# Performance work log

Measured on AMD Instinct MI355X. Metric: run time of the kernel, lower is better.

## Reference

```python
import jax, jax.numpy as jnp
import numpy as np

N = 20000        # nodes
E = 160000       # directed edges (before self loops)
NODE_DIM = 1287
HEADS = 4
C1, C2, C3 = 128, 256, 128
ACT_SLOPE = 0.15   # module's LeakyReLU between layers
GAT_SLOPE = 0.2    # PyG GATConv default negative_slope


def _gat_layer(x, src, dst, W, att_src, att_dst, bias, heads, out_dim, concat):
    # x: [N, in] ; W: [in, heads*out] ; att_*: [heads, out] ; bias: [heads*out] or [out]
    h = (x @ W).reshape(N, heads, out_dim)                      # [N, H, C]
    a_s = jnp.einsum('nhc,hc->nh', h, att_src)                  # [N, H]
    a_d = jnp.einsum('nhc,hc->nh', h, att_dst)                  # [N, H]
    e = jax.nn.leaky_relu(a_s[src] + a_d[dst], GAT_SLOPE)       # [Etot, H]
    # segment softmax over incoming edges of each dst node (self loops => no empty segments)
    m = jax.ops.segment_max(e, dst, num_segments=N)             # [N, H]
    w = jnp.exp(e - m[dst])
    den = jax.ops.segment_sum(w, dst, num_segments=N)           # [N, H]
    alpha = w / den[dst]                                        # [Etot, H]
    msg = h[src] * alpha[:, :, None]                            # [Etot, H, C]
    out = jax.ops.segment_sum(msg, dst, num_segments=N)         # [N, H, C]
    out = out.reshape(N, heads * out_dim) if concat else out.mean(axis=1)
    return out + bias


def setup_inputs() -> dict:
    key = jax.random.key(0)
    ks = jax.random.split(key, 22)
    s = 0.05
    x = jax.random.normal(ks[0], (N, NODE_DIM), jnp.float32)
    edge_index = jax.random.randint(ks[1], (2, E), 0, N, dtype=jnp.int64)
    inp = {
        'x': x, 'edge_index': edge_index,
        'W1': jax.random.normal(ks[2], (NODE_DIM, HEADS * C1), jnp.float32) * s,
        'as1': jax.random.normal(ks[3], (HEADS, C1), jnp.float32) * s,
        'ad1': jax.random.normal(ks[4], (HEADS, C1), jnp.float32) * s,
        'b1': jnp.zeros((HEADS * C1,), jnp.float32),
        'W2': jax.random.normal(ks[5], (HEADS * C1, HEADS * C2), jnp.float32) * s,
        'as2': jax.random.normal(ks[6], (HEADS, C2), jnp.float32) * s,
        'ad2': jax.random.normal(ks[7], (HEADS, C2), jnp.float32) * s,
        'b2': jnp.zeros((HEADS * C2,), jnp.float32),
        # conv3: 1024 -> 128, 1 head, no concat
        'W3': jax.random.normal(ks[8], (HEADS * C2, C3), jnp.float32) * s,
        'as3': jax.random.normal(ks[9], (1, C3), jnp.float32) * s,
        'ad3': jax.random.normal(ks[10], (1, C3), jnp.float32) * s,
        'b3': jnp.zeros((C3,), jnp.float32),
        # pre_fc: 128 -> 16
        'pw': jax.random.normal(ks[11], (C3, 16), jnp.float32) * s,
        'pb': jnp.zeros((16,), jnp.float32),
        # fc fallback: Linear(16,32) -> LeakyReLU(0.15) -> Linear(32,2)
        'f1w': jax.random.normal(ks[12], (16, 32), jnp.float32) * s,
        'f1b': jnp.zeros((32,), jnp.float32),
        'f2w': jax.random.normal(ks[13], (32, 2), jnp.float32) * s,
        'f2b': jnp.zeros((2,), jnp.float32),
    }
    return inp


def reference(x, edge_index, W1, as1, ad1, b1, W2, as2, ad2, b2,
              W3, as3, ad3, b3, pw, pb, f1w, f1b, f2w, f2b):
    loop = jnp.arange(N, dtype=edge_index.dtype)
    src = jnp.concatenate([edge_index[0], loop])   # PyG add_self_loops=True
    dst = jnp.concatenate([edge_index[1], loop])
    h = _gat_layer(x, src, dst, W1, as1, ad1, b1, HEADS, C1, True)
    h = jax.nn.leaky_relu(h, ACT_SLOPE)            # dropout = identity (eval)
    h = _gat_layer(h, src, dst, W2, as2, ad2, b2, HEADS, C2, True)
    h = jax.nn.leaky_relu(h, ACT_SLOPE)
    h = _gat_layer(h, src, dst, W3, as3, ad3, b3, 1, C3, False)
    h = jax.nn.leaky_relu(h, ACT_SLOPE)
    h = h @ pw + pb                                 # pre_fc (128 -> 16)
    h = jax.nn.leaky_relu(h @ f1w + f1b, ACT_SLOPE)
    return h @ f2w + f2b                            # [N, 2] logits
```

## Files before the change

### kernel.cpp

```cpp
#include <hip/hip_runtime.h>
#include <hip/hip_bf16.h>
#include <cstdint>
#include <cstddef>

#define LRELU(x, s) ((x) > 0.f ? (x) : (s) * (x))

typedef __attribute__((ext_vector_type(8))) short bf16x8;
typedef __attribute__((ext_vector_type(4))) float f32x4;

__device__ __forceinline__ float bflo(uint v) { return __uint_as_float(v << 16); }
__device__ __forceinline__ float bfhi(uint v) { return __uint_as_float(v & 0xffff0000u); }
__device__ __forceinline__ ushort f2bf(float f) {
  const uint u = __float_as_uint(f);
  return (ushort)((u + 0x7fffu + ((u >> 16) & 1u)) >> 16);
}

__device__ __forceinline__ void async16(const ushort* g, ushort* l) {
  __builtin_amdgcn_global_load_lds(
      (const __attribute__((address_space(1))) unsigned int*)g,
      (__attribute__((address_space(3))) unsigned int*)l, 16, 0, 0);
}

__global__ void cast_pad_rows(const float* __restrict__ in, ushort* __restrict__ out,
                              int rows, int K, int Kp) {
  const int P4 = Kp >> 2;
  const long long idx = (long long)blockIdx.x * blockDim.x + threadIdx.x;
  if (idx >= (long long)rows * P4) return;
  const int r = (int)(idx / P4);
  const int c = ((int)(idx - (long long)r * P4)) << 2;
  const float* p = in + (size_t)r * K + c;
  float v0 = 0.f, v1 = 0.f, v2 = 0.f, v3 = 0.f;
  if (c + 3 < K) { v0 = p[0]; v1 = p[1]; v2 = p[2]; v3 = p[3]; }
  else {
    if (c + 0 < K) v0 = p[0];
    if (c + 1 < K) v1 = p[1];
    if (c + 2 < K) v2 = p[2];
    if (c + 3 < K) v3 = p[3];
  }
  uint2 o;
  o.x = (uint)f2bf(v0) | ((uint)f2bf(v1) << 16);
  o.y = (uint)f2bf(v2) | ((uint)f2bf(v3) << 16);
  *(uint2*)(out + (size_t)r * Kp + c) = o;
}

__global__ void cast_W_T(const float* __restrict__ W, ushort* __restrict__ Wt,
                         int K, int Nn, int Kp) {
  __shared__ float tile[32][33];
  const int kt = blockIdx.x * 32;
  const int nt = blockIdx.y * 32;
  const int tx = threadIdx.x;
  const int ty = threadIdx.y;
  for (int r = ty; r < 32; r += 8) {
    const int k = kt + r, nn = nt + tx;
    tile[r][tx] = (k < K && nn < Nn) ? W[(size_t)k * Nn + nn] : 0.f;
  }
  __syncthreads();
  for (int r = ty; r < 32; r += 8) {
    const int nn = nt + r, k = kt + tx;
    if (nn < Nn && k < Kp) Wt[(size_t)nn * Kp + k] = f2bf(tile[tx][r]);
  }
}

__global__ __launch_bounds__(256) void gemm_bf16(
    const ushort* __restrict__ A, const ushort* __restrict__ Bt, ushort* __restrict__ C,
    int M, int N, int Kp,
    const float* __restrict__ AS, const float* __restrict__ AD,
    float* __restrict__ asb, float* __restrict__ adb, int H, int headC) {
  __shared__ ushort sA[128 * 32];
  __shared__ ushort sB[128 * 32];
  const int tid = threadIdx.x;
  const int wave = tid >> 6;
  const int lane = tid & 63;
  const int tilesN = N >> 7;
  const int bx = blockIdx.x % tilesN;
  const int by = blockIdx.x / tilesN;
  const int wrow = (wave >> 1) * 64;
  const int wcol = (wave & 1) * 64;
  const int quad = lane >> 4;
  const int ml = lane & 15;

  const int r0 = wave * 32 + (lane >> 2);
  const int r1 = r0 + 16;
  const int seg = (lane & 3) * 8;
  const int gA0 = min(by * 128 + r0, M - 1);
  const int gA1 = min(by * 128 + r1, M - 1);
  const int gB0 = bx * 128 + r0;
  const int gB1 = bx * 128 + r1;
  const ushort* pA0 = A + (size_t)gA0 * Kp + seg;
  const ushort* pA1 = A + (size_t)gA1 * Kp + seg;
  const ushort* pB0 = Bt + (size_t)gB0 * Kp + seg;
  const ushort* pB1 = Bt + (size_t)gB1 * Kp + seg;
  ushort* lA0 = &sA[(wave * 32) * 32];
  ushort* lA1 = &sA[(wave * 32 + 16) * 32];
  ushort* lB0 = &sB[(wave * 32) * 32];
  ushort* lB1 = &sB[(wave * 32 + 16) * 32];

  f32x4 acc[4][4];
#pragma unroll
  for (int mi = 0; mi < 4; mi++)
#pragma unroll
    for (int ni = 0; ni < 4; ni++)
#pragma unroll
      for (int e = 0; e < 4; e++) acc[mi][ni][e] = 0.f;

  for (int k0 = 0; k0 < Kp; k0 += 32) {
    __syncthreads();
    async16(pA0 + k0, lA0);
    async16(pA1 + k0, lA1);
    async16(pB0 + k0, lB0);
    async16(pB1 + k0, lB1);
    __syncthreads();
    bf16x8 af[4], bfr[4];
#pragma unroll
    for (int mi = 0; mi < 4; mi++)
      af[mi] = *(const bf16x8*)&sA[(wrow + mi * 16 + ml) * 32 + quad * 8];
#pragma unroll
    for (int ni = 0; ni < 4; ni++)
      bfr[ni] = *(const bf16x8*)&sB[(wcol + ni * 16 + ml) * 32 + quad * 8];
#pragma unroll
    for (int mi = 0; mi < 4; mi++)
#pragma unroll
      for (int ni = 0; ni < 4; ni++)
        acc[mi][ni] = __builtin_amdgcn_mfma_f32_16x16x32_bf16(af[mi], bfr[ni], acc[mi][ni], 0, 0, 0);
  }

#pragma unroll
  for (int mi = 0; mi < 4; mi++) {
#pragma unroll
    for (int r = 0; r < 4; r++) {
      const int row = by * 128 + wrow + mi * 16 + quad * 4 + r;
      if (row < M) {
#pragma unroll
        for (int ni = 0; ni < 4; ni++) {
          const int col = bx * 128 + wcol + ni * 16 + ml;
          C[(size_t)row * N + col] = f2bf(acc[mi][ni][r]);
        }
      }
    }
  }

  if (asb != nullptr) {
    float asv[4], adv[4];
#pragma unroll
    for (int ni = 0; ni < 4; ni++) {
      const int col = bx * 128 + wcol + ni * 16 + ml;
      asv[ni] = AS[col];
      adv[ni] = AD[col];
    }
    const int hh = (bx * 128 + wcol) / headC;
#pragma unroll
    for (int mi = 0; mi < 4; mi++) {
#pragma unroll
      for (int r = 0; r < 4; r++) {
        float ps = acc[mi][0][r] * asv[0] + acc[mi][1][r] * asv[1] +
                   acc[mi][2][r] * asv[2] + acc[mi][3][r] * asv[3];
        float pd = acc[mi][0][r] * adv[0] + acc[mi][1][r] * adv[1] +
                   acc[mi][2][r] * adv[2] + acc[mi][3][r] * adv[3];
#pragma unroll
        for (int off = 1; off < 16; off <<= 1) {
          ps += __shfl_xor(ps, off);
          pd += __shfl_xor(pd, off);
        }
        if (ml == 0) {
          const int row = by * 128 + wrow + mi * 16 + quad * 4 + r;
          if (row < M) {
            atomicAdd(&asb[row * H + hh], ps);
            atomicAdd(&adb[row * H + hh], pd);
          }
        }
      }
    }
  }
}

__global__ void count_deg(const int* __restrict__ dst, int E, int* __restrict__ deg) {
  const int t = blockIdx.x * blockDim.x + threadIdx.x;
  if (t < E) atomicAdd(&deg[dst[t]], 1);
}

__global__ __launch_bounds__(1024) void scan_kernel(const int* __restrict__ deg,
                                                    int* __restrict__ rowptr,
                                                    int* __restrict__ cursor, int n) {
  __shared__ int swsum[16];
  __shared__ int carry_s;
  const int t = threadIdx.x;
  const int wv = t >> 6, lane = t & 63;
  if (t == 0) carry_s = 0;
  __syncthreads();
  for (int base = 0; base < n; base += 1024) {
    const int i = base + t;
    const int v = (i < n) ? (deg[i] + 1) : 0;
    int sc = v;
#pragma unroll
    for (int off = 1; off < 64; off <<= 1) {
      const int u = __shfl_up(sc, off);
      if (lane >= off) sc += u;
    }
    if (lane == 63) swsum[wv] = sc;
    __syncthreads();
    if (t < 16) {
      int x = swsum[t];
#pragma unroll
      for (int off = 1; off < 16; off <<= 1) {
        const int u = __shfl_up(x, off);
        if (t >= off) x += u;
      }
      swsum[t] = x;
    }
    __syncthreads();
    const int incl = sc + (wv == 0 ? 0 : swsum[wv - 1]) + carry_s;
    if (i < n) { rowptr[i + 1] = incl; cursor[i] = incl - v; }
    if (base == 0 && t == 0) rowptr[0] = 0;
    __syncthreads();
    if (t == 0) carry_s += swsum[15];
    __syncthreads();
  }
}

__global__ void scatter_edges(const int* __restrict__ esrc, const int* __restrict__ edst,
                              int E, int Etot, int* __restrict__ cursor,
                              int* __restrict__ csr_src) {
  const int t = blockIdx.x * blockDim.x + threadIdx.x;
  if (t >= Etot) return;
  int s, d;
  if (t < E) { s = esrc[t]; d = edst[t]; } else { s = t - E; d = s; }
  const int pos = atomicAdd(&cursor[d], 1);
  csr_src[pos] = s;
}

template <int H, int C>
__global__ __launch_bounds__(256) void gat_agg_wave(
    const ushort* __restrict__ hb, const int* __restrict__ rowptr,
    const int* __restrict__ csr_src, const float* __restrict__ a_s,
    const float* __restrict__ a_d, const float* __restrict__ bias,
    ushort* __restrict__ outb, float act_slope, int Nn) {
  constexpr int HC = H * C;
  constexpr int NU = HC / 2;
  constexpr int PPT = NU / 128;
  const int n = blockIdx.x * 4 + (threadIdx.x >> 6);
  const int lane = threadIdx.x & 63;
  if (n >= Nn) return;
  float ad_n[H];
#pragma unroll
  for (int h = 0; h < H; h++) ad_n[h] = a_d[n * H + h];
  const int start = rowptr[n], end = rowptr[n + 1];
  f32x4 acc[PPT];
#pragma unroll
  for (int q = 0; q < PPT; q++)
#pragma unroll
    for (int e = 0; e < 4; e++) acc[q][e] = 0.f;
  float den[H];
#pragma unroll
  for (int h = 0; h < H; h++) den[h] = 0.f;

  for (int base = start; base < end; base += 64) {
    const int cnt = min(64, end - base);
    int s = 0;
    float w[H];
#pragma unroll
    for (int h = 0; h < H; h++) w[h] = 0.f;
    if (lane < cnt) {
      s = csr_src[base + lane];
      float asv[H];
      if constexpr (H == 4) {
        const float4 t4 = *(const float4*)(a_s + s * 4);
        asv[0] = t4.x; asv[1] = t4.y; asv[2] = t4.z; asv[3] = t4.w;
      } else {
        asv[0] = a_s[s];
      }
#pragma unroll
      for (int h = 0; h < H; h++) {
        float lg = asv[h] + ad_n[h];
        lg = LRELU(lg, 0.2f);
        w[h] = __expf(lg);
        den[h] += w[h];
      }
    }
    for (int j = 0; j < cnt; j++) {
      const int sj = __shfl(s, j);
      float wj[H];
#pragma unroll
      for (int h = 0; h < H; h++) wj[h] = __shfl(w[h], j);
      const uint2* hp = (const uint2*)(hb + (size_t)sj * HC);
#pragma unroll
      for (int q = 0; q < PPT; q++) {
        const int pu = q * 128 + lane * 2;
        const uint2 v = hp[q * 64 + lane];
        const float wq = wj[(2 * pu) / C];
        acc[q][0] += wq * bflo(v.x);
        acc[q][1] += wq * bfhi(v.x);
        acc[q][2] += wq * bflo(v.y);
        acc[q][3] += wq * bfhi(v.y);
      }
    }
  }
#pragma unroll
  for (int h = 0; h < H; h++) {
#pragma unroll
    for (int off = 1; off < 64; off <<= 1) den[h] += __shfl_xor(den[h], off);
    den[h] = 1.f / den[h];
  }
#pragma unroll
  for (int q = 0; q < PPT; q++) {
    const int pu = q * 128 + lane * 2;
    const float iv = den[(2 * pu) / C];
    const float4 b4 = *(const float4*)(bias + 2 * pu);
    const float o0 = LRELU(acc[q][0] * iv + b4.x, act_slope);
    const float o1 = LRELU(acc[q][1] * iv + b4.y, act_slope);
    const float o2 = LRELU(acc[q][2] * iv + b4.z, act_slope);
    const float o3 = LRELU(acc[q][3] * iv + b4.w, act_slope);
    uint2 o;
    o.x = (uint)f2bf(o0) | ((uint)f2bf(o1) << 16);
    o.y = (uint)f2bf(o2) | ((uint)f2bf(o3) << 16);
    ((uint2*)outb)[(size_t)n * (NU / 2) + q * 64 + lane] = o;
  }
}

__global__ __launch_bounds__(64) void gat_agg3_mlp(
    const ushort* __restrict__ hb, const int* __restrict__ rowptr,
    const int* __restrict__ csr_src, const float* __restrict__ a_s,
    const float* __restrict__ a_d, const float* __restrict__ b3,
    const float* __restrict__ pw, const float* __restrict__ pb,
    const float* __restrict__ f1w, const float* __restrict__ f1b,
    const float* __restrict__ f2w, const float* __restrict__ f2b,
    float* __restrict__ out) {
  const int n = blockIdx.x;
  const int tid = threadIdx.x;
  __shared__ float sx[128];
  __shared__ float s1[16];
  __shared__ float s2[32];
  const float ad_n = a_d[n];
  const int start = rowptr[n], end = rowptr[n + 1];
  float2 acc = make_float2(0.f, 0.f);
  float den = 0.f;
  for (int base = start; base < end; base += 64) {
    const int cnt = min(64, end - base);
    int s = 0;
    float w = 0.f;
    if (tid < cnt) {
      s = csr_src[base + tid];
      float lg = a_s[s] + ad_n;
      lg = LRELU(lg, 0.2f);
      w = __expf(lg);
      den += w;
    }
    for (int j = 0; j < cnt; j++) {
      const int sj = __shfl(s, j);
      const float wj = __shfl(w, j);
      const uint v = ((const uint*)(hb + (size_t)sj * 128))[tid];
      acc.x += wj * bflo(v);
      acc.y += wj * bfhi(v);
    }
  }
#pragma unroll
  for (int off = 1; off < 64; off <<= 1) den += __shfl_xor(den, off);
  const float iv = 1.f / den;
  sx[2 * tid]     = LRELU(acc.x * iv + b3[2 * tid], 0.15f);
  sx[2 * tid + 1] = LRELU(acc.y * iv + b3[2 * tid + 1], 0.15f);
  __syncthreads();
  if (tid < 16) {
    float a = pb[tid];
    for (int c = 0; c < 128; c++) a += sx[c] * pw[c * 16 + tid];
    s1[tid] = a;
  }
  __syncthreads();
  if (tid < 32) {
    float a = f1b[tid];
    for (int c = 0; c < 16; c++) a += s1[c] * f1w[c * 32 + tid];
    s2[tid] = LRELU(a, 0.15f);
  }
  __syncthreads();
  if (tid < 2) {
    float a = f2b[tid];
    for (int c = 0; c < 32; c++) a += s2[c] * f2w[c * 2 + tid];
    out[(size_t)n * 2 + tid] = a;
  }
}

extern "C" void kernel_launch(void* const* d_in, const int* in_sizes, int n_in,
                              void* d_out, int out_size, void* d_ws, size_t ws_size,
                              hipStream_t stream) {
  const float* x   = (const float*)d_in[0];
  const int* ei    = (const int*)d_in[1];
  const float* W1  = (const float*)d_in[2];
  const float* as1 = (const float*)d_in[3];
  const float* ad1 = (const float*)d_in[4];
  const float* b1  = (const float*)d_in[5];
  const float* W2  = (const float*)d_in[6];
  const float* as2 = (const float*)d_in[7];
  const float* ad2 = (const float*)d_in[8];
  const float* b2  = (const float*)d_in[9];
  const float* W3  = (const float*)d_in[10];
  const float* as3 = (const float*)d_in[11];
  const float* ad3 = (const float*)d_in[12];
  const float* b3  = (const float*)d_in[13];
  const float* pw  = (const float*)d_in[14];
  const float* pb  = (const float*)d_in[15];
  const float* f1w = (const float*)d_in[16];
  const float* f1b = (const float*)d_in[17];
  const float* f2w = (const float*)d_in[18];
  const float* f2b = (const float*)d_in[19];
  float* out = (float*)d_out;

  const int N = in_sizes[0] / 1287;
  const int E = in_sizes[1] / 2;
  const int Etot = E + N;
  const int* esrc = ei;
  const int* edst = ei + E;
  const int K1 = 1287, K1p = 1312;

  char* ws = (char*)d_ws;
  size_t off = 0;
  auto alloc = [&](size_t bytes) -> void* {
    void* p = ws + off;
    off = (off + bytes + 255) & ~(size_t)255;
    return p;
  };
  ushort* hb  = (ushort*)alloc((size_t)N * 1024 * 2);
  ushort* ob  = (ushort*)alloc((size_t)N * 1024 * 2);
  ushort* xb  = (ushort*)alloc((size_t)N * K1p * 2);
  ushort* W1t = (ushort*)alloc((size_t)512 * K1p * 2);
  ushort* W2t = (ushort*)alloc((size_t)1024 * 512 * 2);
  ushort* W3t = (ushort*)alloc((size_t)128 * 1024 * 2);
  float* av   = (float*)alloc((size_t)N * 8 * sizeof(float));
  int* deg    = (int*)alloc((size_t)N * sizeof(int));
  int* rowptr = (int*)alloc((size_t)(N + 1) * sizeof(int));
  int* cursor = (int*)alloc((size_t)N * sizeof(int));
  int* csr    = (int*)alloc((size_t)Etot * sizeof(int));
  float* asb = av;
  float* adb = av + (size_t)N * 4;

  hipMemsetAsync(deg, 0, (size_t)N * sizeof(int), stream);
  count_deg<<<(E + 255) / 256, 256, 0, stream>>>(edst, E, deg);
  scan_kernel<<<1, 1024, 0, stream>>>(deg, rowptr, cursor, N);
  scatter_edges<<<(Etot + 255) / 256, 256, 0, stream>>>(esrc, edst, E, Etot, cursor, csr);

  {
    const long long nx = (long long)N * (K1p / 4);
    cast_pad_rows<<<(int)((nx + 255) / 256), 256, 0, stream>>>(x, xb, N, K1, K1p);
    cast_W_T<<<dim3(K1p / 32, (512 + 31) / 32), dim3(32, 8), 0, stream>>>(W1, W1t, K1, 512, K1p);
    cast_W_T<<<dim3(512 / 32, 1024 / 32), dim3(32, 8), 0, stream>>>(W2, W2t, 512, 1024, 512);
    cast_W_T<<<dim3(1024 / 32, 128 / 32), dim3(32, 8), 0, stream>>>(W3, W3t, 1024, 128, 1024);
  }

  const int tilesM = (N + 127) / 128;
  const int aggBlocks = (N + 3) / 4;

  {
    const int H = 4, C = 128, HC = 512;
    hipMemsetAsync(av, 0, (size_t)N * 8 * sizeof(float), stream);
    gemm_bf16<<<tilesM * (HC / 128), 256, 0, stream>>>(xb, W1t, hb, N, HC, K1p,
                                                       as1, ad1, asb, adb, H, C);
    gat_agg_wave<4, 128><<<aggBlocks, 256, 0, stream>>>(hb, rowptr, csr, asb, adb,
                                                        b1, ob, 0.15f, N);
  }
  {
    const int H = 4, C = 256, HC = 1024;
    hipMemsetAsync(av, 0, (size_t)N * 8 * sizeof(float), stream);
    gemm_bf16<<<tilesM * (HC / 128), 256, 0, stream>>>(ob, W2t, hb, N, HC, 512,
                                                       as2, ad2, asb, adb, H, C);
    gat_agg_wave<4, 256><<<aggBlocks, 256, 0, stream>>>(hb, rowptr, csr, asb, adb,
                                                        b2, ob, 0.15f, N);
  }
  {
    const int HC = 128;
    hipMemsetAsync(av, 0, (size_t)N * 8 * sizeof(float), stream);
    gemm_bf16<<<tilesM * (HC / 128), 256, 0, stream>>>(ob, W3t, hb, N, HC, 1024,
                                                       as3, ad3, asb, adb, 1, 128);
    gat_agg3_mlp<<<N, 64, 0, stream>>>(hb, rowptr, csr, asb, adb, b3,
                                       pw, pb, f1w, f1b, f2w, f2b, out);
  }
}
```

Measured before the change: 542.7 us.

## Double-buffer GEMM LDS loads and use 64-row tiles for layer-3 GEMM

The bf16 MFMA GEMM now double-buffers its LDS tiles. The next K-slice is issued with async global-to-LDS loads while the current slice is computed, and vmcnt waits replace the two full syncthreads per iteration. The kernel is also templated on tile height, and the narrow third-layer GEMM (N=128) launches 64-row tiles so more blocks fill the GPU. This doubles LDS use and depends on the manual waitcnt values being correct for the async loads.

```diff
diff --git a/kernel.cpp b/kernel.cpp
--- a/kernel.cpp
+++ b/kernel.cpp
@@ -20,6 +20,8 @@
       (const __attribute__((address_space(1))) unsigned int*)g,
       (__attribute__((address_space(3))) unsigned int*)l, 16, 0, 0);
 }
+
+#define WAITCNT_VM(n) (0xF70 | (n))
 
 __global__ void cast_pad_rows(const float* __restrict__ in, ushort* __restrict__ out,
                               int rows, int K, int Kp) {
@@ -61,74 +63,102 @@
   }
 }
 
+template <int TM>
 __global__ __launch_bounds__(256) void gemm_bf16(
     const ushort* __restrict__ A, const ushort* __restrict__ Bt, ushort* __restrict__ C,
     int M, int N, int Kp,
     const float* __restrict__ AS, const float* __restrict__ AD,
     float* __restrict__ asb, float* __restrict__ adb, int H, int headC) {
-  __shared__ ushort sA[128 * 32];
-  __shared__ ushort sB[128 * 32];
+  constexpr int MI = TM / 32;
+  constexpr int LPG = (TM == 128) ? 4 : 3;
+  __shared__ ushort sA[2 * TM * 32];
+  __shared__ ushort sB[2 * 128 * 32];
   const int tid = threadIdx.x;
   const int wave = tid >> 6;
   const int lane = tid & 63;
   const int tilesN = N >> 7;
   const int bx = blockIdx.x % tilesN;
   const int by = blockIdx.x / tilesN;
-  const int wrow = (wave >> 1) * 64;
+  const int wrow = (wave >> 1) * (TM / 2);
   const int wcol = (wave & 1) * 64;
   const int quad = lane >> 4;
   const int ml = lane & 15;
 
-  const int r0 = wave * 32 + (lane >> 2);
-  const int r1 = r0 + 16;
   const int seg = (lane & 3) * 8;
-  const int gA0 = min(by * 128 + r0, M - 1);
-  const int gA1 = min(by * 128 + r1, M - 1);
-  const int gB0 = bx * 128 + r0;
-  const int gB1 = bx * 128 + r1;
-  const ushort* pA0 = A + (size_t)gA0 * Kp + seg;
-  const ushort* pA1 = A + (size_t)gA1 * Kp + seg;
+  const int rB0 = wave * 32 + (lane >> 2);
+  const int gB0 = bx * 128 + rB0;
   const ushort* pB0 = Bt + (size_t)gB0 * Kp + seg;
-  const ushort* pB1 = Bt + (size_t)gB1 * Kp + seg;
-  ushort* lA0 = &sA[(wave * 32) * 32];
-  ushort* lA1 = &sA[(wave * 32 + 16) * 32];
+  const ushort* pB1 = Bt + (size_t)(gB0 + 16) * Kp + seg;
   ushort* lB0 = &sB[(wave * 32) * 32];
   ushort* lB1 = &sB[(wave * 32 + 16) * 32];
-
-  f32x4 acc[4][4];
-#pragma unroll
-  for (int mi = 0; mi < 4; mi++)
+  const ushort *pA0, *pA1;
+  ushort *lA0, *lA1;
+  if constexpr (TM == 128) {
+    const int r0 = wave * 32 + (lane >> 2);
+    pA0 = A + (size_t)min(by * TM + r0, M - 1) * Kp + seg;
+    pA1 = A + (size_t)min(by * TM + r0 + 16, M - 1) * Kp + seg;
+    lA0 = &sA[(wave * 32) * 32];
+    lA1 = &sA[(wave * 32 + 16) * 32];
+  } else {
+    const int r0 = wave * 16 + (lane >> 2);
+    pA0 = A + (size_t)min(by * TM + r0, M - 1) * Kp + seg;
+    pA1 = nullptr;
+    lA0 = &sA[(wave * 16) * 32];
+    lA1 = nullptr;
+  }
+
+  const int nIter = Kp >> 5;
+  auto issue = [&](int it, int p) {
+    const int k0 = it << 5;
+    const int oa = p * TM * 32;
+    const int ob_ = p * 128 * 32;
+    async16(pA0 + k0, lA0 + oa);
+    if constexpr (TM == 128) async16(pA1 + k0, lA1 + oa);
+    async16(pB0 + k0, lB0 + ob_);
+    async16(pB1 + k0, lB1 + ob_);
+  };
+
+  f32x4 acc[MI][4];
+#pragma unroll
+  for (int mi = 0; mi < MI; mi++)
 #pragma unroll
     for (int ni = 0; ni < 4; ni++)
 #pragma unroll
       for (int e = 0; e < 4; e++) acc[mi][ni][e] = 0.f;
 
-  for (int k0 = 0; k0 < Kp; k0 += 32) {
-    __syncthreads();
-    async16(pA0 + k0, lA0);
-    async16(pA1 + k0, lA1);
-    async16(pB0 + k0, lB0);
-    async16(pB1 + k0, lB1);
-    __syncthreads();
-    bf16x8 af[4], bfr[4];
-#pragma unroll
-    for (int mi = 0; mi < 4; mi++)
-      af[mi] = *(const bf16x8*)&sA[(wrow + mi * 16 + ml) * 32 + quad * 8];
+  issue(0, 0);
+  if (nIter > 1) issue(1, 1);
+  int p = 0;
+  for (int it = 0; it < nIter; ++it) {
+    if (it + 1 < nIter) __builtin_amdgcn_s_waitcnt(WAITCNT_VM(LPG));
+    else __builtin_amdgcn_s_waitcnt(WAITCNT_VM(0));
+    __builtin_amdgcn_s_barrier();
+    const ushort* bA = &sA[p * TM * 32];
+    const ushort* bB = &sB[p * 128 * 32];
+    bf16x8 af[MI], bfr[4];
+#pragma unroll
+    for (int mi = 0; mi < MI; mi++)
+      af[mi] = *(const bf16x8*)&bA[(wrow + mi * 16 + ml) * 32 + quad * 8];
 #pragma unroll
     for (int ni = 0; ni < 4; ni++)
-      bfr[ni] = *(const bf16x8*)&sB[(wcol + ni * 16 + ml) * 32 + quad * 8];
-#pragma unroll
-    for (int mi = 0; mi < 4; mi++)
+      bfr[ni] = *(const bf16x8*)&bB[(wcol + ni * 16 + ml) * 32 + quad * 8];
+#pragma unroll
+    for (int mi = 0; mi < MI; mi++)
 #pragma unroll
       for (int ni = 0; ni < 4; ni++)
         acc[mi][ni] = __builtin_amdgcn_mfma_f32_16x16x32_bf16(af[mi], bfr[ni], acc[mi][ni], 0, 0, 0);
-  }
-
-#pragma unroll
-  for (int mi = 0; mi < 4; mi++) {
+    if (it + 2 < nIter) {
+      __builtin_amdgcn_s_barrier();
+      issue(it + 2, p);
+    }
+    p ^= 1;
+  }
+
+#pragma unroll
+  for (int mi = 0; mi < MI; mi++) {
 #pragma unroll
     for (int r = 0; r < 4; r++) {
-      const int row = by * 128 + wrow + mi * 16 + quad * 4 + r;
+      const int row = by * TM + wrow + mi * 16 + quad * 4 + r;
       if (row < M) {
 #pragma unroll
         for (int ni = 0; ni < 4; ni++) {
@@ -149,7 +179,7 @@
     }
     const int hh = (bx * 128 + wcol) / headC;
 #pragma unroll
-    for (int mi = 0; mi < 4; mi++) {
+    for (int mi = 0; mi < MI; mi++) {
 #pragma unroll
       for (int r = 0; r < 4; r++) {
         float ps = acc[mi][0][r] * asv[0] + acc[mi][1][r] * asv[1] +
@@ -162,7 +192,7 @@
           pd += __shfl_xor(pd, off);
         }
         if (ml == 0) {
-          const int row = by * 128 + wrow + mi * 16 + quad * 4 + r;
+          const int row = by * TM + wrow + mi * 16 + quad * 4 + r;
           if (row < M) {
             atomicAdd(&asb[row * H + hh], ps);
             atomicAdd(&adb[row * H + hh], pd);
@@ -444,29 +474,30 @@
   }
 
   const int tilesM = (N + 127) / 128;
+  const int tilesM64 = (N + 63) / 64;
   const int aggBlocks = (N + 3) / 4;
 
   {
     const int H = 4, C = 128, HC = 512;
     hipMemsetAsync(av, 0, (size_t)N * 8 * sizeof(float), stream);
-    gemm_bf16<<<tilesM * (HC / 128), 256, 0, stream>>>(xb, W1t, hb, N, HC, K1p,
-                                                       as1, ad1, asb, adb, H, C);
+    gemm_bf16<128><<<tilesM * (HC / 128), 256, 0, stream>>>(xb, W1t, hb, N, HC, K1p,
+                                                            as1, ad1, asb, adb, H, C);
     gat_agg_wave<4, 128><<<aggBlocks, 256, 0, stream>>>(hb, rowptr, csr, asb, adb,
                                                         b1, ob, 0.15f, N);
   }
   {
     const int H = 4, C = 256, HC = 1024;
     hipMemsetAsync(av, 0, (size_t)N * 8 * sizeof(float), stream);
-    gemm_bf16<<<tilesM * (HC / 128), 256, 0, stream>>>(ob, W2t, hb, N, HC, 512,
-                                                       as2, ad2, asb, adb, H, C);
+    gemm_bf16<128><<<tilesM * (HC / 128), 256, 0, stream>>>(ob, W2t, hb, N, HC, 512,
+                                                            as2, ad2, asb, adb, H, C);
     gat_agg_wave<4, 256><<<aggBlocks, 256, 0, stream>>>(hb, rowptr, csr, asb, adb,
                                                         b2, ob, 0.15f, N);
   }
   {
     const int HC = 128;
     hipMemsetAsync(av, 0, (size_t)N * 8 * sizeof(float), stream);
-    gemm_bf16<<<tilesM * (HC / 128), 256, 0, stream>>>(ob, W3t, hb, N, HC, 1024,
-                                                       as3, ad3, asb, adb, 1, 128);
+    gemm_bf16<64><<<tilesM64 * (HC / 128), 256, 0, stream>>>(ob, W3t, hb, N, HC, 1024,
+                                                             as3, ad3, asb, adb, 1, 128);
     gat_agg3_mlp<<<N, 64, 0, stream>>>(hb, rowptr, csr, asb, adb, b3,
                                        pw, pb, f1w, f1b, f2w, f2b, out);
   }
```

Result: faster. 525.6 us (-3.1%).
